# Kernel tuning notes

Measured on AMD Instinct MI355X. Metric: run time of the kernel, lower is better.

## Reference

```python
import jax, jax.numpy as jnp
import numpy as np

NUM_EMBEDDINGS = 1024
EMBEDDING_DIM = 256
COMMITMENT_COST = 0.25


def setup_inputs() -> dict:
    key = jax.random.key(0)
    k1, k2 = jax.random.split(key)
    inputs = jax.random.normal(k1, (64, 32, 32, EMBEDDING_DIM), dtype=jnp.float32)
    embed = jax.random.normal(k2, (NUM_EMBEDDINGS, EMBEDDING_DIM), dtype=jnp.float32)
    return {"inputs": inputs, "embed": embed}


def reference(inputs, embed):
    # Eval-mode forward (no EMA buffer mutation), use_ema=True loss branch.
    input_shape = inputs.shape
    flat = inputs.reshape(-1, EMBEDDING_DIM)  # [N, d]
    distances = (
        jnp.sum(flat * flat, axis=1, keepdims=True)
        + jnp.sum(embed * embed, axis=1)
        - 2.0 * jnp.matmul(flat, embed.T)
    )
    encoding_indices = jnp.argmin(distances, axis=1)  # [N]
    # Gather codebook rows (equivalent to one-hot @ embed)
    quantized = embed[encoding_indices].reshape(input_shape)
    # use_ema branch: loss = commitment * mse(stop_grad(quantized), inputs)
    e_latent_loss = jnp.mean((jax.lax.stop_gradient(quantized) - inputs) ** 2)
    loss = COMMITMENT_COST * e_latent_loss
    # Straight-through estimator
    quantized_st = inputs + jax.lax.stop_gradient(quantized - inputs)
    # Perplexity from code usage histogram (== mean of one-hot encodings)
    n_tokens = flat.shape[0]
    counts = jax.ops.segment_sum(
        jnp.ones((n_tokens,), dtype=jnp.float32), encoding_indices,
        num_segments=NUM_EMBEDDINGS)
    avg_probs = counts / n_tokens
    perplexity = jnp.exp(-jnp.sum(avg_probs * jnp.log(avg_probs + 1e-10)))
    return quantized_st, loss, perplexity, encoding_indices
```

## Files before the change

kernel.cpp:

```cpp
#include <hip/hip_runtime.h>

#define NTOK 65536
#define DIM 256
#define KC 1024
#define EPS 0.08f

typedef __attribute__((ext_vector_type(8))) _Float16 f16x8;
typedef __attribute__((ext_vector_type(4))) float f32x4;

static __device__ __forceinline__ unsigned short f16bits(float f) {
  _Float16 h = (_Float16)f;
  return __builtin_bit_cast(unsigned short, h);
}
static __device__ __forceinline__ void gload16(const void* g, void* l) {
  __builtin_amdgcn_global_load_lds(
      (const __attribute__((address_space(1))) unsigned int*)g,
      (__attribute__((address_space(3))) unsigned int*)l, 16, 0, 0);
}

__global__ __launch_bounds__(256) void vq_prep_e(const float* __restrict__ e,
                                                 unsigned short* __restrict__ eg,
                                                 float* __restrict__ esq,
                                                 int* __restrict__ hist,
                                                 int* __restrict__ fixCount) {
  const int w = threadIdx.x >> 6, l = threadIdx.x & 63;
  const int t = blockIdx.x * 4 + w;
  const float4 v = *reinterpret_cast<const float4*>(&e[t * DIM + l * 4]);
  ushort4 o;
  o.x = f16bits(v.x); o.y = f16bits(v.y); o.z = f16bits(v.z); o.w = f16bits(v.w);
  const int addr = t * 512 + ((l >> 4) << 7) + ((((l & 15) * 8) ^ ((t & 7) << 4)));
  *reinterpret_cast<ushort4*>((char*)eg + addr) = o;
  float s = v.x * v.x + v.y * v.y + v.z * v.z + v.w * v.w;
#pragma unroll
  for (int o2 = 32; o2 > 0; o2 >>= 1) s += __shfl_down(s, o2, 64);
  if (l == 0) esq[t] = s;
  if (blockIdx.x < 4) hist[blockIdx.x * 256 + threadIdx.x] = 0;
  if (blockIdx.x == 0 && threadIdx.x == 0) *fixCount = 0;
}

__global__ __launch_bounds__(256, 2) void vq_argmin_fused(
    const float* __restrict__ x, const unsigned short* __restrict__ eg,
    const float* __restrict__ e, const float* __restrict__ esq,
    float* __restrict__ outIdxF, float* __restrict__ outQ,
    float* __restrict__ bestDist, float* __restrict__ xsq,
    int* __restrict__ hist, int* __restrict__ fixCount,
    int* __restrict__ fixList) {
  __shared__ unsigned short es[3 * 8192];
  __shared__ int fidx[128];

  const int tid = threadIdx.x, lane = tid & 63, w = tid >> 6;
  const int tokBase = blockIdx.x * 128;
  const int col = lane & 15, kq = lane >> 4;

  auto STAGE = [&](int tile, int b) {
    const int ct_ = tile >> 2, kt_ = tile & 3;
#pragma unroll
    for (int q = 0; q < 4; ++q) {
      const int r0 = w * 32 + q * 8;
      const int er = ct_ * 128 + r0 + (lane >> 3);
      gload16(&eg[er * DIM + kt_ * 64 + (lane & 7) * 8], &es[b * 8192 + r0 * 64]);
    }
  };

  STAGE(0, 0);

  f16x8 a[2][8];
  float sqm[2] = {0.f, 0.f};
#pragma unroll
  for (int m = 0; m < 2; ++m) {
#pragma unroll
    for (int s = 0; s < 8; ++s) {
      const float* xp =
          &x[(tokBase + w * 32 + m * 16 + col) * DIM + s * 32 + kq * 8];
      const float4 v0 = *reinterpret_cast<const float4*>(xp);
      const float4 v1 = *reinterpret_cast<const float4*>(xp + 4);
      a[m][s][0] = (_Float16)v0.x; a[m][s][1] = (_Float16)v0.y;
      a[m][s][2] = (_Float16)v0.z; a[m][s][3] = (_Float16)v0.w;
      a[m][s][4] = (_Float16)v1.x; a[m][s][5] = (_Float16)v1.y;
      a[m][s][6] = (_Float16)v1.z; a[m][s][7] = (_Float16)v1.w;
      sqm[m] += v0.x * v0.x + v0.y * v0.y + v0.z * v0.z + v0.w * v0.w +
                v1.x * v1.x + v1.y * v1.y + v1.z * v1.z + v1.w * v1.w;
    }
  }
#pragma unroll
  for (int m = 0; m < 2; ++m) {
    sqm[m] += __shfl_xor(sqm[m], 16, 64);
    sqm[m] += __shfl_xor(sqm[m], 32, 64);
  }
  if (lane < 16) {
    xsq[tokBase + w * 32 + lane] = sqm[0];
    xsq[tokBase + w * 32 + 16 + lane] = sqm[1];
  }

  float best[2][4], second[2][4];
  int bidx[2][4];
#pragma unroll
  for (int mi = 0; mi < 2; ++mi)
#pragma unroll
    for (int r = 0; r < 4; ++r) {
      best[mi][r] = 3.4e38f; second[mi][r] = 3.4e38f; bidx[mi][r] = 0;
    }

  for (int ct = 0; ct < 8; ++ct) {
    f32x4 acc[2][8];
#pragma unroll
    for (int mi = 0; mi < 2; ++mi)
#pragma unroll
      for (int nj = 0; nj < 8; ++nj) acc[mi][nj] = (f32x4){0.f, 0.f, 0.f, 0.f};

#pragma unroll
    for (int kt = 0; kt < 4; ++kt) {
      const int tile = ct * 4 + kt;
      if (tile < 31) {
        STAGE(tile + 1, (tile + 1) % 3);
        asm volatile("s_waitcnt vmcnt(4)" ::: "memory");
      } else {
        asm volatile("s_waitcnt vmcnt(0)" ::: "memory");
      }
      __builtin_amdgcn_s_barrier();
      asm volatile("" ::: "memory");

      const char* bb = (const char*)es + (tile % 3) * 16384;
#pragma unroll
      for (int ks = 0; ks < 2; ++ks) {
        const int kb = ks * 64 + kq * 16;
        f16x8 bfr[8];
#pragma unroll
        for (int nj = 0; nj < 8; ++nj)
          bfr[nj] = *reinterpret_cast<const f16x8*>(
              bb + (nj * 16 + col) * 128 + (kb ^ ((col & 7) << 4)));
#pragma unroll
        for (int mi = 0; mi < 2; ++mi)
#pragma unroll
          for (int nj = 0; nj < 8; ++nj)
            acc[mi][nj] = __builtin_amdgcn_mfma_f32_16x16x32_f16(
                a[mi][kt * 2 + ks], bfr[nj], acc[mi][nj], 0, 0, 0);
      }
    }

#pragma unroll
    for (int nj = 0; nj < 8; ++nj) {
      const int code = ct * 128 + nj * 16 + col;
      const float sqv = esq[code];
#pragma unroll
      for (int mi = 0; mi < 2; ++mi)
#pragma unroll
        for (int r = 0; r < 4; ++r) {
          const float d = fmaf(-2.f, acc[mi][nj][r], sqv);
          if (d < best[mi][r]) {
            second[mi][r] = best[mi][r];
            best[mi][r] = d;
            bidx[mi][r] = code;
          } else if (d < second[mi][r]) {
            second[mi][r] = d;
          }
        }
    }
  }

#pragma unroll
  for (int mi = 0; mi < 2; ++mi)
#pragma unroll
    for (int r = 0; r < 4; ++r) {
      float b = best[mi][r], s2 = second[mi][r];
      int bi = bidx[mi][r];
#pragma unroll
      for (int m = 1; m <= 8; m <<= 1) {
        const float ob = __shfl_xor(b, m, 64);
        const float os = __shfl_xor(s2, m, 64);
        const int   oi = __shfl_xor(bi, m, 64);
        s2 = fminf(fminf(s2, os), fmaxf(b, ob));
        if (ob < b || (ob == b && oi < bi)) { b = ob; bi = oi; }
      }
      if (col == 0) {
        const int tl = w * 32 + mi * 16 + kq * 4 + r;
        const int t = tokBase + tl;
        outIdxF[t] = (float)bi;
        bestDist[t] = b;
        fidx[tl] = bi;
        atomicAdd(&hist[bi], 1);
        if (s2 - b < EPS) {
          const int p = atomicAdd(fixCount, 1);
          fixList[p] = t;
        }
      }
    }
  __syncthreads();

  for (int i = 0; i < 32; ++i) {
    const int id = fidx[w * 32 + i];
    const float4 q = reinterpret_cast<const float4*>(&e[id * DIM])[lane];
    reinterpret_cast<float4*>(&outQ[(tokBase + w * 32 + i) * DIM])[lane] = q;
  }
}

__global__ __launch_bounds__(256) void vq_fixup(
    const float* __restrict__ x, const float* __restrict__ e,
    const float* __restrict__ esq, const int* __restrict__ fixCount,
    const int* __restrict__ fixList, float* __restrict__ outIdxF,
    float* __restrict__ bestDist, float* __restrict__ outQ,
    int* __restrict__ hist) {
  const int n = *fixCount;
  __shared__ float xrow[256];
  __shared__ float rv[4];
  __shared__ int ri[4];
  __shared__ int sOld, sFi;
  const int tid = threadIdx.x;
  for (int it = blockIdx.x; it < n; it += gridDim.x) {
    const int t = fixList[it];
    __syncthreads();
    if (tid < 64) ((float4*)xrow)[tid] = ((const float4*)&x[t * DIM])[tid];
    __syncthreads();
    float bv = 3.4e38f; int bi = 0;
    for (int c = tid; c < KC; c += 256) {
      float s = 0.f;
#pragma unroll
      for (int d = 0; d < DIM; d += 4) {
        const float4 ev = *(const float4*)&e[c * DIM + d];
        s = fmaf(xrow[d], ev.x, s);
        s = fmaf(xrow[d + 1], ev.y, s);
        s = fmaf(xrow[d + 2], ev.z, s);
        s = fmaf(xrow[d + 3], ev.w, s);
      }
      const float dist = fmaf(-2.f, s, esq[c]);
      if (dist < bv) { bv = dist; bi = c; }
    }
#pragma unroll
    for (int m = 1; m <= 32; m <<= 1) {
      const float ob = __shfl_xor(bv, m, 64);
      const int oi = __shfl_xor(bi, m, 64);
      if (ob < bv || (ob == bv && oi < bi)) { bv = ob; bi = oi; }
    }
    const int lane = tid & 63, wv = tid >> 6;
    if (lane == 0) { rv[wv] = bv; ri[wv] = bi; }
    __syncthreads();
    if (tid == 0) {
      float fb = rv[0]; int fi = ri[0];
      for (int k = 1; k < 4; ++k)
        if (rv[k] < fb || (rv[k] == fb && ri[k] < fi)) { fb = rv[k]; fi = ri[k]; }
      sOld = (int)outIdxF[t];
      sFi = fi;
      bestDist[t] = fb;
      if (fi != sOld) {
        atomicSub(&hist[sOld], 1);
        atomicAdd(&hist[fi], 1);
        outIdxF[t] = (float)fi;
      }
    }
    __syncthreads();
    if (sFi != sOld) outQ[t * DIM + tid] = e[sFi * DIM + tid];
    __syncthreads();
  }
}

__global__ __launch_bounds__(1024) void vq_final(
    const int* __restrict__ hist, const float* __restrict__ xsq,
    const float* __restrict__ bestDist, float* __restrict__ outLoss,
    float* __restrict__ outPerp) {
  const int tid = threadIdx.x;
  float ls = 0.f;
  for (int i = 0; i < 64; ++i) {
    const int t = tid + i * 1024;
    ls += xsq[t] + bestDist[t];
  }
  const float p = (float)hist[tid] * (1.f / 65536.f);
  float ent = p * logf(p + 1e-10f);
#pragma unroll
  for (int o = 32; o > 0; o >>= 1) {
    ls += __shfl_down(ls, o, 64);
    ent += __shfl_down(ent, o, 64);
  }
  __shared__ float lbuf[16], ebuf[16];
  const int lane = tid & 63, wv = tid >> 6;
  if (lane == 0) { lbuf[wv] = ls; ebuf[wv] = ent; }
  __syncthreads();
  if (tid == 0) {
    float L = 0.f, E = 0.f;
    for (int i = 0; i < 16; ++i) { L += lbuf[i]; E += ebuf[i]; }
    *outLoss = 0.25f * (L / 16777216.f);
    *outPerp = expf(-E);
  }
}

extern "C" void kernel_launch(void* const* d_in, const int* in_sizes, int n_in,
                              void* d_out, int out_size, void* d_ws, size_t ws_size,
                              hipStream_t stream) {
  const float* x = (const float*)d_in[0];
  const float* e = (const float*)d_in[1];
  float* out = (float*)d_out;
  float* outQ = out;
  float* outLoss = out + 16777216;
  float* outPerp = out + 16777217;
  float* outIdxF = out + 16777218;

  char* ws = (char*)d_ws;
  int*   hist     = (int*)ws;
  float* esq      = (float*)(ws + 4096);
  float* xsq      = (float*)(ws + 8192);
  float* bestDist = (float*)(ws + 270336);
  int*   fixCount = (int*)(ws + 532480);
  int*   fixList  = (int*)(ws + 532496);
  unsigned short* e_f16 = (unsigned short*)(ws + 794640);

  vq_prep_e<<<KC / 4, 256, 0, stream>>>(e, e_f16, esq, hist, fixCount);
  vq_argmin_fused<<<NTOK / 128, 256, 0, stream>>>(
      x, e_f16, e, esq, outIdxF, outQ, bestDist, xsq, hist, fixCount, fixList);
  vq_fixup<<<256, 256, 0, stream>>>(x, e, esq, fixCount, fixList, outIdxF,
                                    bestDist, outQ, hist);
  vq_final<<<1, 1024, 0, stream>>>(hist, xsq, bestDist, outLoss, outPerp);
}
```

Measured before the change: 198.0 us.

## Pre-swizzle f16 codebook into MFMA fragment order and read B directly from global

The codebook prep kernel now writes the f16 codebook in the exact per-lane MFMA B-fragment order, so each lane's 16-byte fragment is contiguous. The argmin kernel drops the LDS triple-buffered staging, its barriers and waitcnts, and loads B fragments straight from global/L2 with fully coalesced vector loads. The 256-thread workgroup barrier before the quantized-row gather is also removed, since each wave now reads only its own fidx entries. This removes LDS traffic and synchronisation but makes every wave refetch the whole 512KB codebook from cache, with no explicit prefetch to hide latency.

```diff
diff --git a/kernel.cpp b/kernel.cpp
--- a/kernel.cpp
+++ b/kernel.cpp
@@ -6,16 +6,12 @@
 #define EPS 0.08f
 
 typedef __attribute__((ext_vector_type(8))) _Float16 f16x8;
+typedef __attribute__((ext_vector_type(8))) unsigned short u16x8;
 typedef __attribute__((ext_vector_type(4))) float f32x4;
 
 static __device__ __forceinline__ unsigned short f16bits(float f) {
   _Float16 h = (_Float16)f;
   return __builtin_bit_cast(unsigned short, h);
-}
-static __device__ __forceinline__ void gload16(const void* g, void* l) {
-  __builtin_amdgcn_global_load_lds(
-      (const __attribute__((address_space(1))) unsigned int*)g,
-      (__attribute__((address_space(3))) unsigned int*)l, 16, 0, 0);
 }
 
 __global__ __launch_bounds__(256) void vq_prep_e(const float* __restrict__ e,
@@ -23,19 +19,25 @@
                                                  float* __restrict__ esq,
                                                  int* __restrict__ hist,
                                                  int* __restrict__ fixCount) {
-  const int w = threadIdx.x >> 6, l = threadIdx.x & 63;
-  const int t = blockIdx.x * 4 + w;
-  const float4 v = *reinterpret_cast<const float4*>(&e[t * DIM + l * 4]);
-  ushort4 o;
-  o.x = f16bits(v.x); o.y = f16bits(v.y); o.z = f16bits(v.z); o.w = f16bits(v.w);
-  const int addr = t * 512 + ((l >> 4) << 7) + ((((l & 15) * 8) ^ ((t & 7) << 4)));
-  *reinterpret_cast<ushort4*>((char*)eg + addr) = o;
-  float s = v.x * v.x + v.y * v.y + v.z * v.z + v.w * v.w;
-#pragma unroll
-  for (int o2 = 32; o2 > 0; o2 >>= 1) s += __shfl_down(s, o2, 64);
-  if (l == 0) esq[t] = s;
+  const int gid = blockIdx.x * 256 + threadIdx.x;
+  const int t = gid >> 5;
+  const int o = gid & 31;
+  const float4 v0 = *reinterpret_cast<const float4*>(&e[t * DIM + o * 8]);
+  const float4 v1 = *reinterpret_cast<const float4*>(&e[t * DIM + o * 8 + 4]);
+  u16x8 u;
+  u[0] = f16bits(v0.x); u[1] = f16bits(v0.y); u[2] = f16bits(v0.z); u[3] = f16bits(v0.w);
+  u[4] = f16bits(v1.x); u[5] = f16bits(v1.y); u[6] = f16bits(v1.z); u[7] = f16bits(v1.w);
+  const int ct = t >> 7, nj = (t >> 4) & 7, col = t & 15;
+  const int s = o >> 2, kq = o & 3;
+  char* dst = (char*)eg + ((ct * 64 + s * 8 + nj) << 10) + ((kq * 16 + col) << 4);
+  *reinterpret_cast<u16x8*>(dst) = u;
+  float p = v0.x * v0.x + v0.y * v0.y + v0.z * v0.z + v0.w * v0.w +
+            v1.x * v1.x + v1.y * v1.y + v1.z * v1.z + v1.w * v1.w;
+#pragma unroll
+  for (int m = 16; m > 0; m >>= 1) p += __shfl_xor(p, m, 64);
+  if (o == 0) esq[t] = p;
   if (blockIdx.x < 4) hist[blockIdx.x * 256 + threadIdx.x] = 0;
-  if (blockIdx.x == 0 && threadIdx.x == 0) *fixCount = 0;
+  if (gid == 0) *fixCount = 0;
 }
 
 __global__ __launch_bounds__(256, 2) void vq_argmin_fused(
@@ -45,24 +47,11 @@
     float* __restrict__ bestDist, float* __restrict__ xsq,
     int* __restrict__ hist, int* __restrict__ fixCount,
     int* __restrict__ fixList) {
-  __shared__ unsigned short es[3 * 8192];
   __shared__ int fidx[128];
 
   const int tid = threadIdx.x, lane = tid & 63, w = tid >> 6;
-  const int tokBase = blockIdx.x * 128;
   const int col = lane & 15, kq = lane >> 4;
-
-  auto STAGE = [&](int tile, int b) {
-    const int ct_ = tile >> 2, kt_ = tile & 3;
-#pragma unroll
-    for (int q = 0; q < 4; ++q) {
-      const int r0 = w * 32 + q * 8;
-      const int er = ct_ * 128 + r0 + (lane >> 3);
-      gload16(&eg[er * DIM + kt_ * 64 + (lane & 7) * 8], &es[b * 8192 + r0 * 64]);
-    }
-  };
-
-  STAGE(0, 0);
+  const int tw = blockIdx.x * 128 + w * 32;
 
   f16x8 a[2][8];
   float sqm[2] = {0.f, 0.f};
@@ -70,8 +59,7 @@
   for (int m = 0; m < 2; ++m) {
 #pragma unroll
     for (int s = 0; s < 8; ++s) {
-      const float* xp =
-          &x[(tokBase + w * 32 + m * 16 + col) * DIM + s * 32 + kq * 8];
+      const float* xp = &x[(tw + m * 16 + col) * DIM + s * 32 + kq * 8];
       const float4 v0 = *reinterpret_cast<const float4*>(xp);
       const float4 v1 = *reinterpret_cast<const float4*>(xp + 4);
       a[m][s][0] = (_Float16)v0.x; a[m][s][1] = (_Float16)v0.y;
@@ -88,8 +76,8 @@
     sqm[m] += __shfl_xor(sqm[m], 32, 64);
   }
   if (lane < 16) {
-    xsq[tokBase + w * 32 + lane] = sqm[0];
-    xsq[tokBase + w * 32 + 16 + lane] = sqm[1];
+    xsq[tw + lane] = sqm[0];
+    xsq[tw + 16 + lane] = sqm[1];
   }
 
   float best[2][4], second[2][4];
@@ -102,6 +90,7 @@
     }
 
   for (int ct = 0; ct < 8; ++ct) {
+    const char* ebase = (const char*)eg + ct * 65536;
     f32x4 acc[2][8];
 #pragma unroll
     for (int mi = 0; mi < 2; ++mi)
@@ -109,33 +98,18 @@
       for (int nj = 0; nj < 8; ++nj) acc[mi][nj] = (f32x4){0.f, 0.f, 0.f, 0.f};
 
 #pragma unroll
-    for (int kt = 0; kt < 4; ++kt) {
-      const int tile = ct * 4 + kt;
-      if (tile < 31) {
-        STAGE(tile + 1, (tile + 1) % 3);
-        asm volatile("s_waitcnt vmcnt(4)" ::: "memory");
-      } else {
-        asm volatile("s_waitcnt vmcnt(0)" ::: "memory");
-      }
-      __builtin_amdgcn_s_barrier();
-      asm volatile("" ::: "memory");
-
-      const char* bb = (const char*)es + (tile % 3) * 16384;
-#pragma unroll
-      for (int ks = 0; ks < 2; ++ks) {
-        const int kb = ks * 64 + kq * 16;
-        f16x8 bfr[8];
+    for (int s = 0; s < 8; ++s) {
+      f16x8 b[8];
+#pragma unroll
+      for (int nj = 0; nj < 8; ++nj)
+        b[nj] = *reinterpret_cast<const f16x8*>(
+            ebase + ((s * 8 + nj) << 10) + (lane << 4));
+#pragma unroll
+      for (int mi = 0; mi < 2; ++mi)
 #pragma unroll
         for (int nj = 0; nj < 8; ++nj)
-          bfr[nj] = *reinterpret_cast<const f16x8*>(
-              bb + (nj * 16 + col) * 128 + (kb ^ ((col & 7) << 4)));
-#pragma unroll
-        for (int mi = 0; mi < 2; ++mi)
-#pragma unroll
-          for (int nj = 0; nj < 8; ++nj)
-            acc[mi][nj] = __builtin_amdgcn_mfma_f32_16x16x32_f16(
-                a[mi][kt * 2 + ks], bfr[nj], acc[mi][nj], 0, 0, 0);
-      }
+          acc[mi][nj] = __builtin_amdgcn_mfma_f32_16x16x32_f16(
+              a[mi][s], b[nj], acc[mi][nj], 0, 0, 0);
     }
 
 #pragma unroll
@@ -174,7 +148,7 @@
       }
       if (col == 0) {
         const int tl = w * 32 + mi * 16 + kq * 4 + r;
-        const int t = tokBase + tl;
+        const int t = tw + mi * 16 + kq * 4 + r;
         outIdxF[t] = (float)bi;
         bestDist[t] = b;
         fidx[tl] = bi;
@@ -185,12 +159,11 @@
         }
       }
     }
-  __syncthreads();
 
   for (int i = 0; i < 32; ++i) {
     const int id = fidx[w * 32 + i];
     const float4 q = reinterpret_cast<const float4*>(&e[id * DIM])[lane];
-    reinterpret_cast<float4*>(&outQ[(tokBase + w * 32 + i) * DIM])[lane] = q;
+    reinterpret_cast<float4*>(&outQ[(tw + i) * DIM])[lane] = q;
   }
 }
 
@@ -302,7 +275,7 @@
   int*   fixList  = (int*)(ws + 532496);
   unsigned short* e_f16 = (unsigned short*)(ws + 794640);
 
-  vq_prep_e<<<KC / 4, 256, 0, stream>>>(e, e_f16, esq, hist, fixCount);
+  vq_prep_e<<<128, 256, 0, stream>>>(e, e_f16, esq, hist, fixCount);
   vq_argmin_fused<<<NTOK / 128, 256, 0, stream>>>(
       x, e_f16, e, esq, outIdxF, outQ, bestDist, xsq, hist, fixCount, fixList);
   vq_fixup<<<256, 256, 0, stream>>>(x, e, esq, fixCount, fixList, outIdxF,
```

Result: slower. 214.0 us (+8.0%).
